# Performance work log

Hardware: AMD Instinct MI355X
Metric: run time of the kernel (lower is better)

## Reference

```python
import jax, jax.numpy as jnp
import numpy as np

B, T, D, H, F = 2048, 256, 32, 256, 256

def setup_inputs() -> dict:
    key = jax.random.key(0)
    ks = jax.random.split(key, 7)
    s = 0.05
    return {
        "obs":  jax.random.normal(ks[0], (B, T, D), dtype=jnp.float32),
        "W_ih": jax.random.normal(ks[1], (4 * H, D), dtype=jnp.float32) * s,
        "W_hh": jax.random.normal(ks[2], (4 * H, H), dtype=jnp.float32) * s,
        "b_ih": jax.random.normal(ks[3], (4 * H,), dtype=jnp.float32) * s,
        "b_hh": jax.random.normal(ks[4], (4 * H,), dtype=jnp.float32) * s,
        "W_fc": jax.random.normal(ks[5], (F, H), dtype=jnp.float32) * s,
        "b_fc": jax.random.normal(ks[6], (F,), dtype=jnp.float32) * s,
    }

def _lstm_last_h(obs, W_ih, W_hh, b_ih, b_hh):
    # Precompute input projections for all timesteps: [T, B, 4H]
    xW = jnp.einsum('btd,gd->tbg', obs, W_ih) + (b_ih + b_hh)
    Hd = W_hh.shape[1]
    h0 = jnp.zeros((obs.shape[0], Hd), obs.dtype)
    c0 = jnp.zeros_like(h0)

    def step(carry, xw_t):
        h, c = carry
        z = xw_t + h @ W_hh.T                      # [B, 4H]
        i, f, g, o = jnp.split(z, 4, axis=-1)      # PyTorch gate order i,f,g,o
        i = jax.nn.sigmoid(i); f = jax.nn.sigmoid(f)
        g = jnp.tanh(g);       o = jax.nn.sigmoid(o)
        c = f * c + i * g
        h = o * jnp.tanh(c)
        return (h, c), None

    (h_last, _), _ = jax.lax.scan(step, (h0, c0), xW)
    return h_last                                  # [B, H]

def reference(obs, W_ih, W_hh, b_ih, b_hh, W_fc, b_fc):
    h_last = _lstm_last_h(obs, W_ih, W_hh, b_ih, b_hh)
    return h_last @ W_fc.T + b_fc                  # [B, F]
```

## Files before the change

kernel.cpp:

```cpp
#include <hip/hip_runtime.h>
#include <stdint.h>


typedef __attribute__((ext_vector_type(8))) short short8;
typedef __attribute__((ext_vector_type(4))) float f32x4;
typedef __attribute__((ext_vector_type(4))) uint32_t u32x4;
typedef unsigned long long ull;

#define LDSTRIDE 296
#define NBT 128

#define BARRIER_LGKM() \
  asm volatile("s_waitcnt lgkmcnt(0)\n\ts_barrier" ::: "memory")

__device__ __forceinline__ short f2bf(float f) {
  uint32_t u = __builtin_bit_cast(uint32_t, f);
  u = (u + 0x7FFFu + ((u >> 16) & 1u)) >> 16;
  return (short)(uint16_t)u;
}

#define LOG2E 1.4426950408889634f
__device__ __forceinline__ float sigmoidf_(float x) {
  return __builtin_amdgcn_rcpf(1.0f + __builtin_amdgcn_exp2f(-LOG2E * x));
}
__device__ __forceinline__ float tanhf_(float x) {
  float t = __builtin_amdgcn_exp2f((2.0f * LOG2E) * x);
  return 1.0f - 2.0f * __builtin_amdgcn_rcpf(t + 1.0f);
}

__device__ __forceinline__ u32x4 load16_sc(const uint32_t* p) {
  u32x4 r;
  asm volatile("global_load_dwordx4 %0, %1, off sc0 sc1\n\ts_waitcnt vmcnt(0)"
               : "=v"(r)
               : "v"(p)
               : "memory");
  return r;
}
__device__ __forceinline__ void store16_sc(uint32_t* p, u32x4 v) {
  asm volatile("global_store_dwordx4 %0, %1, off sc0 sc1" ::"v"(p), "v"(v)
               : "memory");
}

__global__ void zero_xchg(ull* __restrict__ x) {
  size_t i = ((size_t)blockIdx.x * 256 + threadIdx.x) * 4;
  x[i] = 0; x[i + 1] = 0; x[i + 2] = 0; x[i + 3] = 0;
}

__global__ void pack_w(const float* __restrict__ Whh, const float* __restrict__ Wih,
                       short* __restrict__ wpack) {
  int tid = blockIdx.x * 256 + threadIdx.x;
  if (tid >= 576 * 64) return;
  int lane = tid & 63;
  int frag = tid >> 6;
  int g = frag & 3, hu = (frag >> 2) & 7, cg = (frag >> 5) & 1, kt = frag >> 6;
  int n = g * 256 + cg * 128 + hu * 16 + (lane & 15);
  int k0 = kt * 32 + (lane >> 4) * 8;
  short8 v;
#pragma unroll
  for (int j = 0; j < 8; ++j) {
    int k = k0 + j;
    float f = (k < 256) ? Whh[n * 256 + k] : Wih[n * 32 + (k - 256)];
    v[j] = f2bf(f);
  }
  *(short8*)(wpack + (size_t)frag * 512 + lane * 8) = v;
}

__global__ void pack_wfc(const float* __restrict__ Wfc, short* __restrict__ wfc) {
  int tid = blockIdx.x * 256 + threadIdx.x;
  if (tid >= 128 * 64) return;
  int lane = tid & 63;
  int frag = tid >> 6;
  int ct = frag & 15, kt = frag >> 4;
  int n = ct * 16 + (lane & 15);
  int k0 = kt * 32 + (lane >> 4) * 8;
  short8 v;
#pragma unroll
  for (int j = 0; j < 8; ++j) v[j] = f2bf(Wfc[n * 256 + k0 + j]);
  *(short8*)(wfc + (size_t)frag * 512 + lane * 8) = v;
}

#define SLABD(p, c) (((((size_t)(p)) * NBT + bt) * 2 + (c)) * 512 + tid) * 4

__global__ __launch_bounds__(512, 2) void lstm_main(
    const float* __restrict__ obs, const short8* __restrict__ wpack,
    const short8* __restrict__ wfc, const float* __restrict__ b_ih,
    const float* __restrict__ b_hh, const float* __restrict__ b_fc,
    uint32_t* __restrict__ xchg, float* __restrict__ out) {
  __shared__ __align__(16) short A[2][16 * LDSTRIDE];
  const int tid = threadIdx.x;
  const int w = tid >> 6, lane = tid & 63;
  const int l15 = lane & 15, quad = lane >> 4;
  const int bt = blockIdx.x & 127, cg = blockIdx.x >> 7;
  const int row0 = bt * 16;
  const int xr = tid >> 5, xd = tid & 31;
  const int kro = (cg ^ 1) * 4;
  const int klo = cg * 4;

  {
    short* Az = &A[0][0];
    for (int i = tid; i < 2 * 16 * LDSTRIDE; i += 512) Az[i] = 0;
  }

  short8 wfr[9][4];
#pragma unroll
  for (int kt = 0; kt < 9; ++kt)
#pragma unroll
    for (int g = 0; g < 4; ++g)
      wfr[kt][g] = wpack[(size_t)(((kt * 2 + cg) * 8 + w) * 4 + g) * 64 + lane];
#pragma unroll
  for (int kt = 0; kt < 9; ++kt)
#pragma unroll
    for (int g = 0; g < 4; ++g)
      asm volatile("" : "+v"(wfr[kt][g]));

  float bias[4];
#pragma unroll
  for (int g = 0; g < 4; ++g) {
    int idx = g * 256 + cg * 128 + w * 16 + l15;
    bias[g] = b_ih[idx] + b_hh[idx];
  }

  float c4[4];
#pragma unroll
  for (int i = 0; i < 4; ++i) c4[i] = 0.f;

  __syncthreads();
  A[0][xr * LDSTRIDE + 256 + xd] =
      f2bf(obs[((size_t)(row0 + xr) * 256 + 0) * 32 + xd]);
  __syncthreads();

#define MFK(KT)                                                                \
  {                                                                            \
    const short8 a_ =                                                          \
        *(const short8*)&Acur[l15 * LDSTRIDE + (KT)*32 + quad * 8];            \
    acc[0] = __builtin_amdgcn_mfma_f32_16x16x32_bf16(a_, wfr[KT][0], acc[0],   \
                                                     0, 0, 0);                 \
    acc[1] = __builtin_amdgcn_mfma_f32_16x16x32_bf16(a_, wfr[KT][1], acc[1],   \
                                                     0, 0, 0);                 \
    acc[2] = __builtin_amdgcn_mfma_f32_16x16x32_bf16(a_, wfr[KT][2], acc[2],   \
                                                     0, 0, 0);                 \
    acc[3] = __builtin_amdgcn_mfma_f32_16x16x32_bf16(a_, wfr[KT][3], acc[3],   \
                                                     0, 0, 0);                 \
  }

  for (int t = 0; t < 256; ++t) {
    const int p = t & 1;
    short* __restrict__ Acur = &A[p][0];
    short* __restrict__ Anx = &A[p ^ 1][0];
    const int tn = (t < 255) ? (t + 1) : 255;

    const uint32_t* sa = xchg + SLABD(p, cg ^ 1);
    u32x4 sv = (u32x4){0, 0, 0, 0};
    if (t > 0)
      asm volatile("global_load_dwordx4 %0, %1, off sc0 sc1"
                   : "=v"(sv)
                   : "v"(sa)
                   : "memory");

    const float xv = obs[((size_t)(row0 + xr) * 256 + tn) * 32 + xd];

    f32x4 acc[4];
#pragma unroll
    for (int g = 0; g < 4; ++g)
      acc[g] = (f32x4){bias[g], bias[g], bias[g], bias[g]};
    if (cg == 0) { MFK(0) MFK(1) MFK(2) MFK(3) }
    else         { MFK(4) MFK(5) MFK(6) MFK(7) }
    MFK(8)

    if (t > 0) {
      asm volatile("s_waitcnt vmcnt(1)" : "+v"(sv)::"memory");
      __builtin_amdgcn_sched_barrier(0);
      const uint32_t want = (uint32_t)t << 16;
      for (;;) {
        const uint32_t bad = ((sv[0] ^ want) | (sv[1] ^ want) | (sv[2] ^ want) |
                              (sv[3] ^ want)) & 0xFFFF0000u;
        if (!bad) break;
        __builtin_amdgcn_s_sleep(2);
        sv = load16_sc(sa);
      }
      const int scol = kro * 32 + w * 16 + l15;
      Acur[(quad * 4 + 0) * LDSTRIDE + scol] = (short)(uint16_t)sv[0];
      Acur[(quad * 4 + 1) * LDSTRIDE + scol] = (short)(uint16_t)sv[1];
      Acur[(quad * 4 + 2) * LDSTRIDE + scol] = (short)(uint16_t)sv[2];
      Acur[(quad * 4 + 3) * LDSTRIDE + scol] = (short)(uint16_t)sv[3];
    }
    BARRIER_LGKM();

    if (cg == 0) { MFK(4) MFK(5) MFK(6) MFK(7) }
    else         { MFK(0) MFK(1) MFK(2) MFK(3) }

    short hb[4];
#pragma unroll
    for (int reg = 0; reg < 4; ++reg) {
      float iv = sigmoidf_(acc[0][reg]);
      float fv = sigmoidf_(acc[1][reg]);
      float gv = tanhf_(acc[2][reg]);
      float ov = sigmoidf_(acc[3][reg]);
      float cc = fv * c4[reg] + iv * gv;
      c4[reg] = cc;
      hb[reg] = f2bf(ov * tanhf_(cc));
    }

    {
      const uint32_t tg1 = (uint32_t)(t + 1) << 16;
      uint32_t* ds = xchg + SLABD((t + 1) & 1, cg);
      u32x4 pv = (u32x4){tg1 | (uint16_t)hb[0], tg1 | (uint16_t)hb[1],
                         tg1 | (uint16_t)hb[2], tg1 | (uint16_t)hb[3]};
      store16_sc(ds, pv);
    }
    {
      const int ocol = klo * 32 + w * 16 + l15;
#pragma unroll
      for (int reg = 0; reg < 4; ++reg)
        Anx[(quad * 4 + reg) * LDSTRIDE + ocol] = hb[reg];
      Anx[xr * LDSTRIDE + 256 + xd] = f2bf(xv);
    }
    BARRIER_LGKM();
  }
#undef MFK

  {
    const uint32_t* sa = xchg + SLABD(0, cg ^ 1);
    const uint32_t want = 256u << 16;
    u32x4 sv = load16_sc(sa);
    for (;;) {
      const uint32_t bad = ((sv[0] ^ want) | (sv[1] ^ want) | (sv[2] ^ want) |
                            (sv[3] ^ want)) & 0xFFFF0000u;
      if (!bad) break;
      __builtin_amdgcn_s_sleep(2);
      sv = load16_sc(sa);
    }
    const int scol = kro * 32 + w * 16 + l15;
    A[0][(quad * 4 + 0) * LDSTRIDE + scol] = (short)(uint16_t)sv[0];
    A[0][(quad * 4 + 1) * LDSTRIDE + scol] = (short)(uint16_t)sv[1];
    A[0][(quad * 4 + 2) * LDSTRIDE + scol] = (short)(uint16_t)sv[2];
    A[0][(quad * 4 + 3) * LDSTRIDE + scol] = (short)(uint16_t)sv[3];
  }
  __syncthreads();

  {
    const int ct = cg * 8 + w;
    const int col = ct * 16 + l15;
    const float bv = b_fc[col];
    f32x4 ao = (f32x4){0.f, 0.f, 0.f, 0.f};
#pragma unroll
    for (int kt = 0; kt < 8; ++kt) {
      const short8 a = *(const short8*)&A[0][l15 * LDSTRIDE + kt * 32 + quad * 8];
      const short8 b = wfc[(size_t)(kt * 16 + ct) * 64 + lane];
      ao = __builtin_amdgcn_mfma_f32_16x16x32_bf16(a, b, ao, 0, 0, 0);
    }
#pragma unroll
    for (int reg = 0; reg < 4; ++reg) {
      const int row = row0 + quad * 4 + reg;
      out[(size_t)row * 256 + col] = ao[reg] + bv;
    }
  }
}

extern "C" void kernel_launch(void* const* d_in, const int* in_sizes, int n_in,
                              void* d_out, int out_size, void* d_ws, size_t ws_size,
                              hipStream_t stream) {
  const float* obs  = (const float*)d_in[0];
  const float* W_ih = (const float*)d_in[1];
  const float* W_hh = (const float*)d_in[2];
  const float* b_ih = (const float*)d_in[3];
  const float* b_hh = (const float*)d_in[4];
  const float* W_fc = (const float*)d_in[5];
  const float* b_fc = (const float*)d_in[6];
  float* out = (float*)d_out;

  short*    wpack = (short*)d_ws;
  short*    wfcp  = wpack + 576 * 512;
  uint32_t* xchg  = (uint32_t*)((char*)d_ws + (576 + 128) * 1024);

  hipLaunchKernelGGL(zero_xchg, dim3(512), dim3(256), 0, stream, (ull*)xchg);
  hipLaunchKernelGGL(pack_w, dim3(144), dim3(256), 0, stream, W_hh, W_ih, wpack);
  hipLaunchKernelGGL(pack_wfc, dim3(32), dim3(256), 0, stream, W_fc, wfcp);
  hipLaunchKernelGGL(lstm_main, dim3(256), dim3(512), 0, stream, obs,
                     (const short8*)wpack, (const short8*)wfcp,
                     b_ih, b_hh, b_fc, xchg, out);
}
```

Baseline: 557.6 us.

## Process two batch tiles per block to overlap cross-block exchange latency

Each workgroup now owns two 16-row batch tiles instead of one, and the grid shrinks from 256 to 128 blocks. Within each timestep the two tiles' recurrent MFMA, gate math and global hidden-state exchange are interleaved, so the partner block's handoff for one tile can arrive while the other tile computes. The aim is to hide the per-step global-memory exchange and spin-wait latency that dominates the serial recurrence. The cost is twice the per-block work per step, half as many active CUs, extra LDS buffers and more barriers per step.

After: 883.4 us. +58.4%, slower.

```diff
diff --git a/kernel.cpp b/kernel.cpp
--- a/kernel.cpp
+++ b/kernel.cpp
@@ -79,26 +79,28 @@
   *(short8*)(wfc + (size_t)frag * 512 + lane * 8) = v;
 }
 
-#define SLABD(p, c) (((((size_t)(p)) * NBT + bt) * 2 + (c)) * 512 + tid) * 4
+#define SLABD(p, c, BT) \
+  ((((((size_t)(p)) * NBT + (BT)) * 2 + (c)) * 512 + tid) * 4)
 
 __global__ __launch_bounds__(512, 2) void lstm_main(
     const float* __restrict__ obs, const short8* __restrict__ wpack,
     const short8* __restrict__ wfc, const float* __restrict__ b_ih,
     const float* __restrict__ b_hh, const float* __restrict__ b_fc,
     uint32_t* __restrict__ xchg, float* __restrict__ out) {
-  __shared__ __align__(16) short A[2][16 * LDSTRIDE];
+  __shared__ __align__(16) short A[2][2][16 * LDSTRIDE];
   const int tid = threadIdx.x;
   const int w = tid >> 6, lane = tid & 63;
   const int l15 = lane & 15, quad = lane >> 4;
-  const int bt = blockIdx.x & 127, cg = blockIdx.x >> 7;
-  const int row0 = bt * 16;
+  const int pairid = blockIdx.x & 63, cg = blockIdx.x >> 6;
+  const int bt0 = pairid * 2, bt1 = bt0 + 1;
+  const int row0 = bt0 * 16, row1 = bt1 * 16;
   const int xr = tid >> 5, xd = tid & 31;
   const int kro = (cg ^ 1) * 4;
   const int klo = cg * 4;
 
   {
-    short* Az = &A[0][0];
-    for (int i = tid; i < 2 * 16 * LDSTRIDE; i += 512) Az[i] = 0;
+    short* Az = &A[0][0][0];
+    for (int i = tid; i < 2 * 2 * 16 * LDSTRIDE; i += 512) Az[i] = 0;
   }
 
   short8 wfr[9][4];
@@ -120,13 +122,15 @@
     bias[g] = b_ih[idx] + b_hh[idx];
   }
 
-  float c4[4];
-#pragma unroll
-  for (int i = 0; i < 4; ++i) c4[i] = 0.f;
+  float c0s[4], c1s[4];
+#pragma unroll
+  for (int i = 0; i < 4; ++i) { c0s[i] = 0.f; c1s[i] = 0.f; }
 
   __syncthreads();
-  A[0][xr * LDSTRIDE + 256 + xd] =
+  A[0][0][xr * LDSTRIDE + 256 + xd] =
       f2bf(obs[((size_t)(row0 + xr) * 256 + 0) * 32 + xd]);
+  A[1][0][xr * LDSTRIDE + 256 + xd] =
+      f2bf(obs[((size_t)(row1 + xr) * 256 + 0) * 32 + xd]);
   __syncthreads();
 
 #define MFK(KT)                                                                \
@@ -145,82 +149,149 @@
 
   for (int t = 0; t < 256; ++t) {
     const int p = t & 1;
-    short* __restrict__ Acur = &A[p][0];
-    short* __restrict__ Anx = &A[p ^ 1][0];
+    short* __restrict__ A0c = &A[0][p][0];
+    short* __restrict__ A0n = &A[0][p ^ 1][0];
+    short* __restrict__ A1c = &A[1][p][0];
+    short* __restrict__ A1n = &A[1][p ^ 1][0];
     const int tn = (t < 255) ? (t + 1) : 255;
 
-    const uint32_t* sa = xchg + SLABD(p, cg ^ 1);
-    u32x4 sv = (u32x4){0, 0, 0, 0};
-    if (t > 0)
+    const uint32_t* sa0 = xchg + SLABD(p, cg ^ 1, bt0);
+    const uint32_t* sa1 = xchg + SLABD(p, cg ^ 1, bt1);
+    u32x4 sv0 = (u32x4){0, 0, 0, 0}, sv1 = (u32x4){0, 0, 0, 0};
+    if (t > 0) {
       asm volatile("global_load_dwordx4 %0, %1, off sc0 sc1"
-                   : "=v"(sv)
-                   : "v"(sa)
-                   : "memory");
-
-    const float xv = obs[((size_t)(row0 + xr) * 256 + tn) * 32 + xd];
-
-    f32x4 acc[4];
-#pragma unroll
-    for (int g = 0; g < 4; ++g)
-      acc[g] = (f32x4){bias[g], bias[g], bias[g], bias[g]};
-    if (cg == 0) { MFK(0) MFK(1) MFK(2) MFK(3) }
-    else         { MFK(4) MFK(5) MFK(6) MFK(7) }
-    MFK(8)
-
-    if (t > 0) {
-      asm volatile("s_waitcnt vmcnt(1)" : "+v"(sv)::"memory");
-      __builtin_amdgcn_sched_barrier(0);
-      const uint32_t want = (uint32_t)t << 16;
-      for (;;) {
-        const uint32_t bad = ((sv[0] ^ want) | (sv[1] ^ want) | (sv[2] ^ want) |
-                              (sv[3] ^ want)) & 0xFFFF0000u;
-        if (!bad) break;
-        __builtin_amdgcn_s_sleep(2);
-        sv = load16_sc(sa);
-      }
-      const int scol = kro * 32 + w * 16 + l15;
-      Acur[(quad * 4 + 0) * LDSTRIDE + scol] = (short)(uint16_t)sv[0];
-      Acur[(quad * 4 + 1) * LDSTRIDE + scol] = (short)(uint16_t)sv[1];
-      Acur[(quad * 4 + 2) * LDSTRIDE + scol] = (short)(uint16_t)sv[2];
-      Acur[(quad * 4 + 3) * LDSTRIDE + scol] = (short)(uint16_t)sv[3];
-    }
+                   : "=v"(sv0) : "v"(sa0) : "memory");
+      asm volatile("global_load_dwordx4 %0, %1, off sc0 sc1"
+                   : "=v"(sv1) : "v"(sa1) : "memory");
+    }
+    const float xv0 = obs[((size_t)(row0 + xr) * 256 + tn) * 32 + xd];
+    const float xv1 = obs[((size_t)(row1 + xr) * 256 + tn) * 32 + xd];
+
+    {
+      short* __restrict__ Acur = A0c;
+      f32x4 acc[4];
+#pragma unroll
+      for (int g = 0; g < 4; ++g)
+        acc[g] = (f32x4){bias[g], bias[g], bias[g], bias[g]};
+      if (cg == 0) { MFK(0) MFK(1) MFK(2) MFK(3) }
+      else         { MFK(4) MFK(5) MFK(6) MFK(7) }
+      MFK(8)
+
+      if (t > 0) {
+        asm volatile("s_waitcnt vmcnt(3)" : "+v"(sv0)::"memory");
+        __builtin_amdgcn_sched_barrier(0);
+        const uint32_t want = (uint32_t)t << 16;
+        for (;;) {
+          const uint32_t bad =
+              ((sv0[0] ^ want) | (sv0[1] ^ want) | (sv0[2] ^ want) |
+               (sv0[3] ^ want)) & 0xFFFF0000u;
+          if (!bad) break;
+          __builtin_amdgcn_s_sleep(2);
+          sv0 = load16_sc(sa0);
+        }
+        const int scol = kro * 32 + w * 16 + l15;
+        A0c[(quad * 4 + 0) * LDSTRIDE + scol] = (short)(uint16_t)sv0[0];
+        A0c[(quad * 4 + 1) * LDSTRIDE + scol] = (short)(uint16_t)sv0[1];
+        A0c[(quad * 4 + 2) * LDSTRIDE + scol] = (short)(uint16_t)sv0[2];
+        A0c[(quad * 4 + 3) * LDSTRIDE + scol] = (short)(uint16_t)sv0[3];
+      }
+      BARRIER_LGKM();
+
+      if (cg == 0) { MFK(4) MFK(5) MFK(6) MFK(7) }
+      else         { MFK(0) MFK(1) MFK(2) MFK(3) }
+
+      short hb[4];
+#pragma unroll
+      for (int reg = 0; reg < 4; ++reg) {
+        float iv = sigmoidf_(acc[0][reg]);
+        float fv = sigmoidf_(acc[1][reg]);
+        float gv = tanhf_(acc[2][reg]);
+        float ov = sigmoidf_(acc[3][reg]);
+        float cc = fv * c0s[reg] + iv * gv;
+        c0s[reg] = cc;
+        hb[reg] = f2bf(ov * tanhf_(cc));
+      }
+      {
+        const uint32_t tg1 = (uint32_t)(t + 1) << 16;
+        u32x4 pv = (u32x4){tg1 | (uint16_t)hb[0], tg1 | (uint16_t)hb[1],
+                           tg1 | (uint16_t)hb[2], tg1 | (uint16_t)hb[3]};
+        store16_sc(xchg + SLABD((t + 1) & 1, cg, bt0), pv);
+      }
+      {
+        const int ocol = klo * 32 + w * 16 + l15;
+#pragma unroll
+        for (int reg = 0; reg < 4; ++reg)
+          A0n[(quad * 4 + reg) * LDSTRIDE + ocol] = hb[reg];
+      }
+    }
+
+    {
+      short* __restrict__ Acur = A1c;
+      f32x4 acc[4];
+#pragma unroll
+      for (int g = 0; g < 4; ++g)
+        acc[g] = (f32x4){bias[g], bias[g], bias[g], bias[g]};
+      if (cg == 0) { MFK(0) MFK(1) MFK(2) MFK(3) }
+      else         { MFK(4) MFK(5) MFK(6) MFK(7) }
+      MFK(8)
+
+      if (t > 0) {
+        asm volatile("s_waitcnt vmcnt(1)" : "+v"(sv1)::"memory");
+        __builtin_amdgcn_sched_barrier(0);
+        const uint32_t want = (uint32_t)t << 16;
+        for (;;) {
+          const uint32_t bad =
+              ((sv1[0] ^ want) | (sv1[1] ^ want) | (sv1[2] ^ want) |
+               (sv1[3] ^ want)) & 0xFFFF0000u;
+          if (!bad) break;
+          __builtin_amdgcn_s_sleep(2);
+          sv1 = load16_sc(sa1);
+        }
+        const int scol = kro * 32 + w * 16 + l15;
+        A1c[(quad * 4 + 0) * LDSTRIDE + scol] = (short)(uint16_t)sv1[0];
+        A1c[(quad * 4 + 1) * LDSTRIDE + scol] = (short)(uint16_t)sv1[1];
+        A1c[(quad * 4 + 2) * LDSTRIDE + scol] = (short)(uint16_t)sv1[2];
+        A1c[(quad * 4 + 3) * LDSTRIDE + scol] = (short)(uint16_t)sv1[3];
+      }
+      BARRIER_LGKM();
+
+      if (cg == 0) { MFK(4) MFK(5) MFK(6) MFK(7) }
+      else         { MFK(0) MFK(1) MFK(2) MFK(3) }
+
+      short hb[4];
+#pragma unroll
+      for (int reg = 0; reg < 4; ++reg) {
+        float iv = sigmoidf_(acc[0][reg]);
+        float fv = sigmoidf_(acc[1][reg]);
+        float gv = tanhf_(acc[2][reg]);
+        float ov = sigmoidf_(acc[3][reg]);
+        float cc = fv * c1s[reg] + iv * gv;
+        c1s[reg] = cc;
+        hb[reg] = f2bf(ov * tanhf_(cc));
+      }
+      {
+        const uint32_t tg1 = (uint32_t)(t + 1) << 16;
+        u32x4 pv = (u32x4){tg1 | (uint16_t)hb[0], tg1 | (uint16_t)hb[1],
+                           tg1 | (uint16_t)hb[2], tg1 | (uint16_t)hb[3]};
+        store16_sc(xchg + SLABD((t + 1) & 1, cg, bt1), pv);
+      }
+      {
+        const int ocol = klo * 32 + w * 16 + l15;
+#pragma unroll
+        for (int reg = 0; reg < 4; ++reg)
+          A1n[(quad * 4 + reg) * LDSTRIDE + ocol] = hb[reg];
+      }
+    }
+
+    A0n[xr * LDSTRIDE + 256 + xd] = f2bf(xv0);
+    A1n[xr * LDSTRIDE + 256 + xd] = f2bf(xv1);
     BARRIER_LGKM();
-
-    if (cg == 0) { MFK(4) MFK(5) MFK(6) MFK(7) }
-    else         { MFK(0) MFK(1) MFK(2) MFK(3) }
-
-    short hb[4];
-#pragma unroll
-    for (int reg = 0; reg < 4; ++reg) {
-      float iv = sigmoidf_(acc[0][reg]);
-      float fv = sigmoidf_(acc[1][reg]);
-      float gv = tanhf_(acc[2][reg]);
-      float ov = sigmoidf_(acc[3][reg]);
-      float cc = fv * c4[reg] + iv * gv;
-      c4[reg] = cc;
-      hb[reg] = f2bf(ov * tanhf_(cc));
-    }
-
-    {
-      const uint32_t tg1 = (uint32_t)(t + 1) << 16;
-      uint32_t* ds = xchg + SLABD((t + 1) & 1, cg);
-      u32x4 pv = (u32x4){tg1 | (uint16_t)hb[0], tg1 | (uint16_t)hb[1],
-                         tg1 | (uint16_t)hb[2], tg1 | (uint16_t)hb[3]};
-      store16_sc(ds, pv);
-    }
-    {
-      const int ocol = klo * 32 + w * 16 + l15;
-#pragma unroll
-      for (int reg = 0; reg < 4; ++reg)
-        Anx[(quad * 4 + reg) * LDSTRIDE + ocol] = hb[reg];
-      Anx[xr * LDSTRIDE + 256 + xd] = f2bf(xv);
-    }
-    BARRIER_LGKM();
   }
 #undef MFK
 
-  {
-    const uint32_t* sa = xchg + SLABD(0, cg ^ 1);
+#pragma unroll
+  for (int ti = 0; ti < 2; ++ti) {
+    const uint32_t* sa = xchg + SLABD(0, cg ^ 1, (ti ? bt1 : bt0));
     const uint32_t want = 256u << 16;
     u32x4 sv = load16_sc(sa);
     for (;;) {
@@ -231,10 +302,11 @@
       sv = load16_sc(sa);
     }
     const int scol = kro * 32 + w * 16 + l15;
-    A[0][(quad * 4 + 0) * LDSTRIDE + scol] = (short)(uint16_t)sv[0];
-    A[0][(quad * 4 + 1) * LDSTRIDE + scol] = (short)(uint16_t)sv[1];
-    A[0][(quad * 4 + 2) * LDSTRIDE + scol] = (short)(uint16_t)sv[2];
-    A[0][(quad * 4 + 3) * LDSTRIDE + scol] = (short)(uint16_t)sv[3];
+    short* Af = &A[ti][0][0];
+    Af[(quad * 4 + 0) * LDSTRIDE + scol] = (short)(uint16_t)sv[0];
+    Af[(quad * 4 + 1) * LDSTRIDE + scol] = (short)(uint16_t)sv[1];
+    Af[(quad * 4 + 2) * LDSTRIDE + scol] = (short)(uint16_t)sv[2];
+    Af[(quad * 4 + 3) * LDSTRIDE + scol] = (short)(uint16_t)sv[3];
   }
   __syncthreads();
 
@@ -242,17 +314,20 @@
     const int ct = cg * 8 + w;
     const int col = ct * 16 + l15;
     const float bv = b_fc[col];
-    f32x4 ao = (f32x4){0.f, 0.f, 0.f, 0.f};
-#pragma unroll
-    for (int kt = 0; kt < 8; ++kt) {
-      const short8 a = *(const short8*)&A[0][l15 * LDSTRIDE + kt * 32 + quad * 8];
-      const short8 b = wfc[(size_t)(kt * 16 + ct) * 64 + lane];
-      ao = __builtin_amdgcn_mfma_f32_16x16x32_bf16(a, b, ao, 0, 0, 0);
-    }
-#pragma unroll
-    for (int reg = 0; reg < 4; ++reg) {
-      const int row = row0 + quad * 4 + reg;
-      out[(size_t)row * 256 + col] = ao[reg] + bv;
+#pragma unroll
+    for (int ti = 0; ti < 2; ++ti) {
+      const short* Af = &A[ti][0][0];
+      f32x4 ao = (f32x4){0.f, 0.f, 0.f, 0.f};
+#pragma unroll
+      for (int kt = 0; kt < 8; ++kt) {
+        const short8 a = *(const short8*)&Af[l15 * LDSTRIDE + kt * 32 + quad * 8];
+        const short8 b = wfc[(size_t)(kt * 16 + ct) * 64 + lane];
+        ao = __builtin_amdgcn_mfma_f32_16x16x32_bf16(a, b, ao, 0, 0, 0);
+      }
+      const int rbase = (ti ? row1 : row0) + quad * 4;
+#pragma unroll
+      for (int reg = 0; reg < 4; ++reg)
+        out[(size_t)(rbase + reg) * 256 + col] = ao[reg] + bv;
     }
   }
 }
@@ -276,7 +351,7 @@
   hipLaunchKernelGGL(zero_xchg, dim3(512), dim3(256), 0, stream, (ull*)xchg);
   hipLaunchKernelGGL(pack_w, dim3(144), dim3(256), 0, stream, W_hh, W_ih, wpack);
   hipLaunchKernelGGL(pack_wfc, dim3(32), dim3(256), 0, stream, W_fc, wfcp);
-  hipLaunchKernelGGL(lstm_main, dim3(256), dim3(512), 0, stream, obs,
+  hipLaunchKernelGGL(lstm_main, dim3(128), dim3(512), 0, stream, obs,
                      (const short8*)wpack, (const short8*)wfcp,
                      b_ih, b_hh, b_fc, xchg, out);
 }
```
